# Kernel tuning notes

Measured on AMD Instinct MI355X. Metric: run time of the kernel, lower is better.

The kernel has to match this reference:

```python
import jax, jax.numpy as jnp
import numpy as np

B, N_LAT, N_PAT = 32, 64, 4096
DIM_LAT = DIM_PAT = DIM_ATTN = 192
H = 6
HD = DIM_ATTN // H  # 32
SCALE = HD ** -0.5


def setup_inputs() -> dict:
    key = jax.random.key(0)
    ks = jax.random.split(key, 8)
    s = lambda fan_in: 1.0 / np.sqrt(fan_in)
    return {
        "x_latents": jax.random.normal(ks[0], (B, N_LAT, DIM_LAT), jnp.float32),
        "x_patches": jax.random.normal(ks[1], (B, N_PAT, DIM_PAT), jnp.float32),
        # weights stored [in, out] (torch Linear applies x @ W.T; math identical)
        "W_rv_lat": jax.random.uniform(ks[2], (DIM_LAT, 2 * DIM_ATTN), jnp.float32, -s(DIM_LAT), s(DIM_LAT)),
        "W_rv_pat": jax.random.uniform(ks[3], (DIM_PAT, 2 * DIM_ATTN), jnp.float32, -s(DIM_PAT), s(DIM_PAT)),
        "W_proj_lat": jax.random.uniform(ks[4], (DIM_ATTN, DIM_LAT), jnp.float32, -s(DIM_ATTN), s(DIM_ATTN)),
        "b_proj_lat": jax.random.uniform(ks[5], (DIM_LAT,), jnp.float32, -s(DIM_ATTN), s(DIM_ATTN)),
        "W_proj_pat": jax.random.uniform(ks[6], (DIM_ATTN, DIM_PAT), jnp.float32, -s(DIM_ATTN), s(DIM_ATTN)),
        "b_proj_pat": jax.random.uniform(ks[7], (DIM_PAT,), jnp.float32, -s(DIM_ATTN), s(DIM_ATTN)),
    }


def _split_rv(x, W, n):
    # x: [B, n, d_in] -> r, v each [B, H, n, HD]
    rv = (x @ W).reshape(x.shape[0], n, 2, H, HD)
    rv = jnp.transpose(rv, (2, 0, 3, 1, 4))  # [2, B, H, n, HD]
    return rv[0], rv[1]


def reference(x_latents, x_patches, W_rv_lat, W_rv_pat,
              W_proj_lat, b_proj_lat, W_proj_pat, b_proj_pat):
    r_lat, v_lat = _split_rv(x_latents, W_rv_lat, N_LAT)   # [B,H,N_lat,HD]
    r_pat, v_pat = _split_rv(x_patches, W_rv_pat, N_PAT)   # [B,H,N_pat,HD]

    # single score matrix, softmaxed along both axes (dropout = 0, eval mode)
    scores = jnp.einsum('bhld,bhpd->bhlp', r_lat, r_pat) * SCALE  # [B,H,N_lat,N_pat]
    attn = jax.nn.softmax(scores, axis=-1)    # row-wise (over patches)
    attn_T = jax.nn.softmax(scores, axis=-2)  # col-wise (over latents)

    out_lat = jnp.einsum('bhlp,bhpd->blhd', attn, v_pat).reshape(B, N_LAT, DIM_ATTN)
    out_pat = jnp.einsum('bhlp,bhld->bphd', attn_T, v_lat).reshape(B, N_PAT, DIM_ATTN)

    out_lat = out_lat @ W_proj_lat + b_proj_lat
    out_pat = out_pat @ W_proj_pat + b_proj_pat
    return out_lat, out_pat
```

## Files before the change

kernel.cpp:

```cpp
#include <hip/hip_runtime.h>

#define B_   32
#define NL_  64
#define NP_  4096
#define DIM_ 192
#define H_   6
#define HD_  32
#define PC_  128
#define NCH_ (NP_/PC_)
#define CPB_ 4
#define NSC_ (NCH_/CPB_)

typedef unsigned short u16;
typedef __attribute__((ext_vector_type(8))) short bf16x8;
typedef __attribute__((ext_vector_type(4))) short bf16x4;
typedef __attribute__((ext_vector_type(4))) float f32x4;

#define MFMA16(a,b,c) __builtin_amdgcn_mfma_f32_16x16x32_bf16(a,b,c,0,0,0)

__device__ __forceinline__ float bf2f(u16 s){ return __builtin_bit_cast(float,(unsigned)s<<16); }
__device__ __forceinline__ u16 f2bf(float f){
  unsigned u = __builtin_bit_cast(unsigned,f);
  return (u16)((u + 0x7FFFu + ((u>>16)&1u))>>16);
}

__global__ void k0_transpose(const float* __restrict__ W0, const float* __restrict__ W1,
                             const float* __restrict__ W2, const float* __restrict__ W3,
                             u16* __restrict__ T0, u16* __restrict__ T1,
                             u16* __restrict__ T2, u16* __restrict__ T3){
  int m = blockIdx.x >> 4, sub = blockIdx.x & 15;
  const float* src; u16* dst; int R, C;
  if      (m==0){src=W0;dst=T0;R=192;C=384;}
  else if (m==1){src=W1;dst=T1;R=192;C=384;}
  else if (m==2){src=W2;dst=T2;R=192;C=192;}
  else          {src=W3;dst=T3;R=192;C=192;}
  int total = R*C;
  for (int o = sub*256 + threadIdx.x; o < total; o += 16*256){
    int c = o / R, r = o - c*R;
    dst[o] = f2bf(src[r*C + c]);
  }
}

__global__ __launch_bounds__(512,2) void k_rv(const float* __restrict__ X,
    const u16* __restrict__ Wt, u16* __restrict__ R, u16* __restrict__ V,
    int Nseq, int nshift){
  __shared__ u16 Bs[2][64*200];
  const int t = threadIdx.x;
  const int m0 = blockIdx.x*256;
  const int lane = t & 63, w = t >> 6, g = lane >> 4, ln = lane & 15;
  const int srB = t >> 3, bq = t & 7;
  const f32x4 ZF = {0.f,0.f,0.f,0.f};

  bf16x8 af[2][6];
  #pragma unroll
  for (int i=0;i<2;i++)
    #pragma unroll
    for (int kk=0;kk<6;kk++){
      const float* s = &X[(size_t)(m0 + w*32 + i*16 + ln)*192 + kk*32 + g*8];
      float4 x0 = *(const float4*)s;
      float4 x1 = *(const float4*)(s+4);
      bf16x8 v;
      v[0]=(short)f2bf(x0.x); v[1]=(short)f2bf(x0.y); v[2]=(short)f2bf(x0.z); v[3]=(short)f2bf(x0.w);
      v[4]=(short)f2bf(x1.x); v[5]=(short)f2bf(x1.y); v[6]=(short)f2bf(x1.z); v[7]=(short)f2bf(x1.w);
      af[i][kk] = v;
    }

  bf16x8 breg[3];
  #pragma unroll
  for (int it=0; it<3; it++)
    breg[it] = *(const bf16x8*)&Wt[(size_t)srB*192 + bq*24 + it*8];
  #pragma unroll
  for (int it=0; it<3; it++)
    *(bf16x8*)&Bs[0][srB*200 + bq*24 + it*8] = breg[it];
  #pragma unroll
  for (int it=0; it<3; it++)
    breg[it] = *(const bf16x8*)&Wt[(size_t)(64 + srB)*192 + bq*24 + it*8];
  __syncthreads();

  for (int c = 0; c < 6; ++c){
    if (c < 5){
      u16* bn = &Bs[(c+1)&1][0];
      #pragma unroll
      for (int it=0; it<3; it++)
        *(bf16x8*)&bn[srB*200 + bq*24 + it*8] = breg[it];
      if (c < 4){
        #pragma unroll
        for (int it=0; it<3; it++)
          breg[it] = *(const bf16x8*)&Wt[(size_t)((c+2)*64 + srB)*192 + bq*24 + it*8];
      }
    }
    const u16* bc = &Bs[c&1][0];
    f32x4 accT[4][2];
    #pragma unroll
    for(int j=0;j<4;j++){ accT[j][0]=ZF; accT[j][1]=ZF; }
    #pragma unroll
    for (int kk=0; kk<6; kk++)
      #pragma unroll
      for (int j=0; j<4; j++){
        bf16x8 bv = *(const bf16x8*)&bc[(j*16 + ln)*200 + kk*32 + g*8];
        accT[j][0] = MFMA16(bv, af[0][kk], accT[j][0]);
        accT[j][1] = MFMA16(bv, af[1][kk], accT[j][1]);
      }
    #pragma unroll
    for(int j=0;j<4;j++){
      int nb = c*64 + j*16 + g*4;
      u16* dst; int cc;
      if (nb < 192){ dst = R; cc = nb; } else { dst = V; cc = nb - 192; }
      int h = cc >> 5, d0 = cc & 31;
      #pragma unroll
      for(int i=0;i<2;i++){
        int m = m0 + w*32 + i*16 + ln;
        int b = m >> nshift, sidx = m & (Nseq-1);
        bf16x4 pk;
        #pragma unroll
        for(int r=0;r<4;r++) pk[r] = (short)f2bf(accT[j][i][r]);
        *(bf16x4*)&dst[((((size_t)b*H_ + h)*(size_t)Nseq + sidx) << 5) + d0] = pk;
      }
    }
    __syncthreads();
  }
}

__global__ __launch_bounds__(256) void k_attn(
    const u16* __restrict__ r_lat_g, const u16* __restrict__ v_lat_g,
    const u16* __restrict__ r_pat_g, const u16* __restrict__ v_pat_g,
    u16* __restrict__ Opat,
    float* __restrict__ numT_ws,
    float* __restrict__ rowsum_ws){
  const float SCALE = 0.17677669529663687f;
  const int sc = blockIdx.x, h = blockIdx.y, b = blockIdx.z;
  const int bh = b*H_ + h;
  const int t = threadIdx.x, lane = t&63, w = t>>6, g = lane>>4, ln = lane&15;
  __shared__ u16 RL [64*40];
  __shared__ u16 VLT[32*72];
  __shared__ u16 EN [128*72];
  __shared__ u16 ET [64*136];
  __shared__ float RS[4*64];
  __shared__ u16 POOL[128*40];
  u16* RP  = POOL;
  u16* VPT = POOL;
  const f32x4 ZF = {0.f,0.f,0.f,0.f};

  const size_t latbase = (size_t)bh * (NL_*HD_);
  { int row = t>>2, col = (t&3)*8;
    *(bf16x8*)&RL[row*40+col] = *(const bf16x8*)&r_lat_g[latbase + row*32 + col]; }
  { int l = t>>2, dd = (t&3)*8;
    bf16x8 v = *(const bf16x8*)&v_lat_g[latbase + l*32 + dd];
    #pragma unroll
    for(int jj=0;jj<8;jj++) VLT[(dd+jj)*72 + l] = (u16)v[jj]; }

  const int p0 = t>>2, dd0 = (t&3)*8;
  const size_t pb0 = ((size_t)bh*NP_ + (size_t)sc*(CPB_*PC_))*HD_;
  bf16x8 rcur0 = *(const bf16x8*)&r_pat_g[pb0 + (size_t)p0*32 + dd0];
  bf16x8 rcur1 = *(const bf16x8*)&r_pat_g[pb0 + (size_t)(64+p0)*32 + dd0];
  bf16x8 vcur0 = *(const bf16x8*)&v_pat_g[pb0 + (size_t)p0*32 + dd0];
  bf16x8 vcur1 = *(const bf16x8*)&v_pat_g[pb0 + (size_t)(64+p0)*32 + dd0];

  f32x4 nmT[2]; nmT[0]=ZF; nmT[1]=ZF;
  float rs[4] = {0.f,0.f,0.f,0.f};

  for (int c = 0; c < CPB_; ++c){
    *(bf16x8*)&RP[p0*40 + dd0]      = rcur0;
    *(bf16x8*)&RP[(64+p0)*40 + dd0] = rcur1;
    __syncthreads();

    f32x4 sf[2][4];
    { bf16x8 a0 = *(const bf16x8*)&RP[(w*32      + ln)*40 + g*8];
      bf16x8 a1 = *(const bf16x8*)&RP[(w*32 + 16 + ln)*40 + g*8];
      #pragma unroll
      for(int j=0;j<4;j++){
        bf16x8 bl = *(const bf16x8*)&RL[(j*16 + ln)*40 + g*8];
        sf[0][j] = MFMA16(a0, bl, ZF);
        sf[1][j] = MFMA16(a1, bl, ZF);
      } }

    bf16x8 rnxt0, rnxt1, vnxt0, vnxt1;
    const bool more = (c+1 < CPB_);
    if (more){
      const size_t pbn = pb0 + (size_t)(c+1)*(PC_*HD_);
      rnxt0 = *(const bf16x8*)&r_pat_g[pbn + (size_t)p0*32 + dd0];
      rnxt1 = *(const bf16x8*)&r_pat_g[pbn + (size_t)(64+p0)*32 + dd0];
      vnxt0 = *(const bf16x8*)&v_pat_g[pbn + (size_t)p0*32 + dd0];
      vnxt1 = *(const bf16x8*)&v_pat_g[pbn + (size_t)(64+p0)*32 + dd0];
    }

    float e[2][4][4], rcs[2][4];
    #pragma unroll
    for(int i=0;i<2;i++)
      #pragma unroll
      for(int r=0;r<4;r++){
        float cs = 0.f;
        #pragma unroll
        for(int j=0;j<4;j++){
          float ev = __expf(sf[i][j][r] * SCALE);
          e[i][j][r] = ev; cs += ev; rs[j] += ev;
        }
        cs += __shfl_xor(cs,1); cs += __shfl_xor(cs,2);
        cs += __shfl_xor(cs,4); cs += __shfl_xor(cs,8);
        rcs[i][r] = 1.0f / cs;
      }
    #pragma unroll
    for(int i=0;i<2;i++)
      #pragma unroll
      for(int j=0;j<4;j++){
        #pragma unroll
        for(int r=0;r<4;r++)
          EN[(w*32 + i*16 + g*4 + r)*72 + j*16 + ln] = f2bf(e[i][j][r]*rcs[i][r]);
        bf16x4 pk;
        #pragma unroll
        for(int r=0;r<4;r++) pk[r] = (short)f2bf(e[i][j][r]);
        *(bf16x4*)&ET[(j*16+ln)*136 + w*32 + i*16 + g*4] = pk;
      }

    f32x4 opT[2][2];
    #pragma unroll
    for(int jd=0;jd<2;jd++){ opT[jd][0]=ZF; opT[jd][1]=ZF; }
    #pragma unroll
    for(int ks=0; ks<2; ks++){
      bf16x8 bv[2];
      #pragma unroll
      for(int jd=0;jd<2;jd++) bv[jd] = *(const bf16x8*)&VLT[(jd*16+ln)*72 + ks*32 + g*8];
      #pragma unroll
      for(int i=0;i<2;i++){
        bf16x8 afen = *(const bf16x8*)&EN[(w*32 + i*16 + ln)*72 + ks*32 + g*8];
        #pragma unroll
        for(int jd=0;jd<2;jd++) opT[jd][i] = MFMA16(bv[jd], afen, opT[jd][i]);
      }
    }
    const size_t obase = ((size_t)b*NP_ + (size_t)(sc*CPB_ + c)*PC_)*DIM_ + h*32;
    #pragma unroll
    for(int jd=0;jd<2;jd++)
      #pragma unroll
      for(int i=0;i<2;i++){
        int p = w*32 + i*16 + ln, d0 = jd*16 + g*4;
        bf16x4 pk;
        #pragma unroll
        for(int r=0;r<4;r++) pk[r] = (short)f2bf(opT[jd][i][r]);
        *(bf16x4*)&Opat[obase + (size_t)p*DIM_ + d0] = pk;
      }
    __syncthreads();

    #pragma unroll
    for(int jj=0;jj<8;jj++){
      VPT[(dd0+jj)*136 + p0]      = (u16)vcur0[jj];
      VPT[(dd0+jj)*136 + 64 + p0] = (u16)vcur1[jj];
    }
    __syncthreads();

    #pragma unroll
    for(int ks=0; ks<4; ks++){
      bf16x8 afet = *(const bf16x8*)&ET[(w*16+ln)*136 + ks*32 + g*8];
      #pragma unroll
      for(int dj=0;dj<2;dj++){
        bf16x8 bv = *(const bf16x8*)&VPT[(dj*16+ln)*136 + ks*32 + g*8];
        nmT[dj] = MFMA16(bv, afet, nmT[dj]);
      }
    }
    __syncthreads();

    if (more){ rcur0=rnxt0; rcur1=rnxt1; vcur0=vnxt0; vcur1=vnxt1; }
  }

  #pragma unroll
  for(int j=0;j<4;j++){
    float vs = rs[j];
    vs += __shfl_xor(vs,16); vs += __shfl_xor(vs,32);
    if (g == 0) RS[w*64 + j*16 + ln] = vs;
  }
  __syncthreads();
  if (t < 64)
    rowsum_ws[((size_t)bh*NSC_ + sc)*64 + t] = RS[t] + RS[64+t] + RS[128+t] + RS[192+t];
  float* dstN = numT_ws + ((size_t)bh*NSC_ + sc)*2048;
  #pragma unroll
  for(int dj=0;dj<2;dj++){
    int l = w*16 + ln, d0 = dj*16 + g*4;
    *(f32x4*)&dstN[l*32 + d0] = nmT[dj];
  }
}

__global__ __launch_bounds__(256) void k_lat_reduce(const float* __restrict__ numT_ws,
    const float* __restrict__ rowsum_ws, u16* __restrict__ attn_lat){
  int bh = blockIdx.x, b = bh / H_, h = bh - b*H_;
  __shared__ float RSs[64];
  int t = threadIdx.x;
  if (t < 64){
    float s = 0.f;
    for(int c=0;c<NSC_;c++) s += rowsum_ws[((size_t)bh*NSC_ + c)*64 + t];
    RSs[t] = 1.0f / s;
  }
  __syncthreads();
  for(int idx = t; idx < 2048; idx += 256){
    int l = idx >> 5, dd = idx & 31;
    float s = 0.f;
    for(int c=0;c<NSC_;c++) s += numT_ws[((size_t)bh*NSC_ + c)*2048 + idx];
    attn_lat[((size_t)b*NL_ + l)*DIM_ + h*32 + dd] = f2bf(s * RSs[l]);
  }
}

__global__ __launch_bounds__(256) void k_proj_lat(const u16* __restrict__ A,
    const u16* __restrict__ Wt, const float* __restrict__ bias, float* __restrict__ out){
  int b = blockIdx.x;
  __shared__ u16 As[64*40];
  __shared__ u16 Bs[192*40];
  int t = threadIdx.x, lane = t&63, w = t>>6, g = lane>>4, ln = lane&15;
  const f32x4 ZF = {0.f,0.f,0.f,0.f};
  f32x4 acc[4][3];
  #pragma unroll
  for(int i=0;i<4;i++)
    #pragma unroll
    for(int j=0;j<3;j++) acc[i][j]=ZF;
  for(int k0=0;k0<192;k0+=32){
    bf16x8 av; bf16x8 bv[3];
    { int row = t>>2, col=(t&3)*8;
      av = *(const bf16x8*)&A[((size_t)b*NL_ + row)*DIM_ + k0 + col]; }
    #pragma unroll
    for(int it=0;it<3;it++){
      int e = it*2048 + t*8, row = e>>5, col = (t&3)*8;
      bv[it] = *(const bf16x8*)&Wt[(size_t)row*192 + k0 + col];
    }
    if (k0) __syncthreads();
    { int row = t>>2, col=(t&3)*8; *(bf16x8*)&As[row*40+col] = av; }
    #pragma unroll
    for(int it=0;it<3;it++){
      int e = it*2048 + t*8, row = e>>5, col = (t&3)*8;
      *(bf16x8*)&Bs[row*40+col] = bv[it];
    }
    __syncthreads();
    bf16x8 bw[3];
    #pragma unroll
    for(int jf=0;jf<3;jf++) bw[jf] = *(const bf16x8*)&Bs[(w*48 + jf*16 + ln)*40 + g*8];
    #pragma unroll
    for(int lf=0;lf<4;lf++){
      bf16x8 af = *(const bf16x8*)&As[(lf*16 + ln)*40 + g*8];
      #pragma unroll
      for(int jf=0;jf<3;jf++) acc[lf][jf] = MFMA16(af, bw[jf], acc[lf][jf]);
    }
  }
  #pragma unroll
  for(int lf=0;lf<4;lf++)
    #pragma unroll
    for(int jf=0;jf<3;jf++){
      int j = w*48 + jf*16 + ln;
      float bs = bias[j];
      #pragma unroll
      for(int r=0;r<4;r++){
        int l = lf*16 + g*4 + r;
        out[((size_t)b*NL_ + l)*DIM_ + j] = acc[lf][jf][r] + bs;
      }
    }
}

__global__ __launch_bounds__(512,2) void k_proj_pat(const u16* __restrict__ X,
    const u16* __restrict__ Wt, const float* __restrict__ bias, float* __restrict__ out){
  __shared__ u16 Bs[2][64*200];
  const int t = threadIdx.x;
  const int m0 = blockIdx.x*256;
  const int lane = t & 63, w = t >> 6, g = lane >> 4, ln = lane & 15;
  const int srB = t >> 3, bq = t & 7;
  const f32x4 ZF = {0.f,0.f,0.f,0.f};

  bf16x8 af[2][6];
  #pragma unroll
  for (int i=0;i<2;i++)
    #pragma unroll
    for (int kk=0;kk<6;kk++)
      af[i][kk] = *(const bf16x8*)&X[(size_t)(m0 + w*32 + i*16 + ln)*192 + kk*32 + g*8];

  bf16x8 breg[3];
  #pragma unroll
  for (int it=0; it<3; it++)
    breg[it] = *(const bf16x8*)&Wt[(size_t)srB*192 + bq*24 + it*8];
  #pragma unroll
  for (int it=0; it<3; it++)
    *(bf16x8*)&Bs[0][srB*200 + bq*24 + it*8] = breg[it];
  #pragma unroll
  for (int it=0; it<3; it++)
    breg[it] = *(const bf16x8*)&Wt[(size_t)(64 + srB)*192 + bq*24 + it*8];
  __syncthreads();

  for (int c = 0; c < 3; ++c){
    if (c < 2){
      u16* bn = &Bs[(c+1)&1][0];
      #pragma unroll
      for (int it=0; it<3; it++)
        *(bf16x8*)&bn[srB*200 + bq*24 + it*8] = breg[it];
      if (c < 1){
        #pragma unroll
        for (int it=0; it<3; it++)
          breg[it] = *(const bf16x8*)&Wt[(size_t)((c+2)*64 + srB)*192 + bq*24 + it*8];
      }
    }
    const u16* bc = &Bs[c&1][0];
    f32x4 accT[4][2];
    #pragma unroll
    for(int j=0;j<4;j++){ accT[j][0]=ZF; accT[j][1]=ZF; }
    #pragma unroll
    for (int kk=0; kk<6; kk++)
      #pragma unroll
      for (int j=0; j<4; j++){
        bf16x8 bv = *(const bf16x8*)&bc[(j*16 + ln)*200 + kk*32 + g*8];
        accT[j][0] = MFMA16(bv, af[0][kk], accT[j][0]);
        accT[j][1] = MFMA16(bv, af[1][kk], accT[j][1]);
      }
    #pragma unroll
    for(int j=0;j<4;j++){
      int nb = c*64 + j*16 + g*4;
      float4 bs4 = *(const float4*)&bias[nb];
      #pragma unroll
      for(int i=0;i<2;i++){
        int m = m0 + w*32 + i*16 + ln;
        float4 o;
        o.x = accT[j][i][0] + bs4.x;
        o.y = accT[j][i][1] + bs4.y;
        o.z = accT[j][i][2] + bs4.z;
        o.w = accT[j][i][3] + bs4.w;
        *(float4*)&out[(size_t)m*192 + nb] = o;
      }
    }
    __syncthreads();
  }
}

extern "C" void kernel_launch(void* const* d_in, const int* in_sizes, int n_in,
                              void* d_out, int out_size, void* d_ws, size_t ws_size,
                              hipStream_t stream){
  const float* x_lat  = (const float*)d_in[0];
  const float* x_pat  = (const float*)d_in[1];
  const float* W_rv_l = (const float*)d_in[2];
  const float* W_rv_p = (const float*)d_in[3];
  const float* W_pj_l = (const float*)d_in[4];
  const float* b_pj_l = (const float*)d_in[5];
  const float* W_pj_p = (const float*)d_in[6];
  const float* b_pj_p = (const float*)d_in[7];
  float* out = (float*)d_out;

  char* ws = (char*)d_ws;
  size_t off = 0;
  auto alloc = [&](size_t bytes)->void*{ void* p = ws + off; off += (bytes + 255) & ~(size_t)255; return p; };
  u16* WtRL   = (u16*)alloc((size_t)384*192*2);
  u16* WtRP   = (u16*)alloc((size_t)384*192*2);
  u16* WtPL   = (u16*)alloc((size_t)192*192*2);
  u16* WtPP   = (u16*)alloc((size_t)192*192*2);
  u16* r_lat  = (u16*)alloc((size_t)B_*H_*NL_*HD_*2);
  u16* v_lat  = (u16*)alloc((size_t)B_*H_*NL_*HD_*2);
  u16* r_pat  = (u16*)alloc((size_t)B_*H_*NP_*HD_*2);
  u16* v_pat  = (u16*)alloc((size_t)B_*H_*NP_*HD_*2);
  u16* Opat   = (u16*)alloc((size_t)B_*NP_*DIM_*2);
  float* numT = (float*)alloc((size_t)B_*H_*NSC_*64*32*4);
  float* rsum = (float*)alloc((size_t)B_*H_*NSC_*64*4);
  u16* attn_l = (u16*)alloc((size_t)B_*NL_*DIM_*2);

  k0_transpose<<<64,256,0,stream>>>(W_rv_l, W_rv_p, W_pj_l, W_pj_p, WtRL, WtRP, WtPL, WtPP);
  k_rv<<<dim3((B_*NP_)/256),512,0,stream>>>(x_pat, WtRP, r_pat, v_pat, NP_, 12);
  k_rv<<<dim3((B_*NL_)/256),512,0,stream>>>(x_lat, WtRL, r_lat, v_lat, NL_, 6);
  k_attn<<<dim3(NSC_, H_, B_),256,0,stream>>>(r_lat, v_lat, r_pat, v_pat, Opat, numT, rsum);
  k_lat_reduce<<<B_*H_,256,0,stream>>>(numT, rsum, attn_l);
  k_proj_lat<<<B_,256,0,stream>>>(attn_l, WtPL, b_pj_l, out);
  k_proj_pat<<<dim3((B_*NP_)/256),512,0,stream>>>(Opat, WtPP, b_pj_p, out + (size_t)B_*NL_*DIM_);
}
```

Before: 177.4 us.

## Pre-swizzle weights into MFMA fragment order and read them directly from global

The weight transpose kernel now writes the rv and patch-projection weights in the exact per-lane MFMA fragment order, so each lane loads its B-operand with one contiguous 16-byte global read. The LDS double-buffering, staging loads and per-chunk barriers in k_rv and k_proj_pat are removed. Blocks shrink to 256 threads covering 128 rows, with 4 blocks per CU. This removes shared-memory traffic and synchronisation, but every wave now re-reads the small weight matrix from L1/L2 instead of sharing one LDS copy.

```diff
diff --git a/kernel.cpp b/kernel.cpp
--- a/kernel.cpp
+++ b/kernel.cpp
@@ -29,26 +29,34 @@
                              u16* __restrict__ T0, u16* __restrict__ T1,
                              u16* __restrict__ T2, u16* __restrict__ T3){
   int m = blockIdx.x >> 4, sub = blockIdx.x & 15;
-  const float* src; u16* dst; int R, C;
-  if      (m==0){src=W0;dst=T0;R=192;C=384;}
-  else if (m==1){src=W1;dst=T1;R=192;C=384;}
-  else if (m==2){src=W2;dst=T2;R=192;C=192;}
-  else          {src=W3;dst=T3;R=192;C=192;}
-  int total = R*C;
+  if (m == 2){
+    for (int o = sub*256 + threadIdx.x; o < 192*192; o += 16*256){
+      int n = o / 192, k = o - n*192;
+      T2[o] = f2bf(W2[k*192 + n]);
+    }
+    return;
+  }
+  const float* src; u16* dst; int NF, C;
+  if      (m==0){src=W0;dst=T0;NF=144;C=384;}
+  else if (m==1){src=W1;dst=T1;NF=144;C=384;}
+  else          {src=W3;dst=T3;NF=72; C=192;}
+  int total = NF*512;
   for (int o = sub*256 + threadIdx.x; o < total; o += 16*256){
-    int c = o / R, r = o - c*R;
-    dst[o] = f2bf(src[r*C + c]);
-  }
-}
-
-__global__ __launch_bounds__(512,2) void k_rv(const float* __restrict__ X,
-    const u16* __restrict__ Wt, u16* __restrict__ R, u16* __restrict__ V,
+    int e = o & 7, l = (o >> 3) & 63, f = o >> 9;
+    int kk = f % 6, jc = f / 6;
+    int j = jc & 3, c = jc >> 2;
+    int n = c*64 + j*16 + (l & 15);
+    int k = kk*32 + (l >> 4)*8 + e;
+    dst[o] = f2bf(src[k*C + n]);
+  }
+}
+
+__global__ __launch_bounds__(256,4) void k_rv(const float* __restrict__ X,
+    const u16* __restrict__ Wf, u16* __restrict__ R, u16* __restrict__ V,
     int Nseq, int nshift){
-  __shared__ u16 Bs[2][64*200];
   const int t = threadIdx.x;
-  const int m0 = blockIdx.x*256;
+  const int m0 = blockIdx.x*128;
   const int lane = t & 63, w = t >> 6, g = lane >> 4, ln = lane & 15;
-  const int srB = t >> 3, bq = t & 7;
   const f32x4 ZF = {0.f,0.f,0.f,0.f};
 
   bf16x8 af[2][6];
@@ -65,31 +73,7 @@
       af[i][kk] = v;
     }
 
-  bf16x8 breg[3];
-  #pragma unroll
-  for (int it=0; it<3; it++)
-    breg[it] = *(const bf16x8*)&Wt[(size_t)srB*192 + bq*24 + it*8];
-  #pragma unroll
-  for (int it=0; it<3; it++)
-    *(bf16x8*)&Bs[0][srB*200 + bq*24 + it*8] = breg[it];
-  #pragma unroll
-  for (int it=0; it<3; it++)
-    breg[it] = *(const bf16x8*)&Wt[(size_t)(64 + srB)*192 + bq*24 + it*8];
-  __syncthreads();
-
   for (int c = 0; c < 6; ++c){
-    if (c < 5){
-      u16* bn = &Bs[(c+1)&1][0];
-      #pragma unroll
-      for (int it=0; it<3; it++)
-        *(bf16x8*)&bn[srB*200 + bq*24 + it*8] = breg[it];
-      if (c < 4){
-        #pragma unroll
-        for (int it=0; it<3; it++)
-          breg[it] = *(const bf16x8*)&Wt[(size_t)((c+2)*64 + srB)*192 + bq*24 + it*8];
-      }
-    }
-    const u16* bc = &Bs[c&1][0];
     f32x4 accT[4][2];
     #pragma unroll
     for(int j=0;j<4;j++){ accT[j][0]=ZF; accT[j][1]=ZF; }
@@ -97,7 +81,7 @@
     for (int kk=0; kk<6; kk++)
       #pragma unroll
       for (int j=0; j<4; j++){
-        bf16x8 bv = *(const bf16x8*)&bc[(j*16 + ln)*200 + kk*32 + g*8];
+        bf16x8 bv = *(const bf16x8*)&Wf[(size_t)(((c*4 + j)*6 + kk) << 9) + lane*8];
         accT[j][0] = MFMA16(bv, af[0][kk], accT[j][0]);
         accT[j][1] = MFMA16(bv, af[1][kk], accT[j][1]);
       }
@@ -117,7 +101,6 @@
         *(bf16x4*)&dst[((((size_t)b*H_ + h)*(size_t)Nseq + sidx) << 5) + d0] = pk;
       }
     }
-    __syncthreads();
   }
 }
 
@@ -350,13 +333,11 @@
     }
 }
 
-__global__ __launch_bounds__(512,2) void k_proj_pat(const u16* __restrict__ X,
-    const u16* __restrict__ Wt, const float* __restrict__ bias, float* __restrict__ out){
-  __shared__ u16 Bs[2][64*200];
+__global__ __launch_bounds__(256,4) void k_proj_pat(const u16* __restrict__ X,
+    const u16* __restrict__ Wf, const float* __restrict__ bias, float* __restrict__ out){
   const int t = threadIdx.x;
-  const int m0 = blockIdx.x*256;
+  const int m0 = blockIdx.x*128;
   const int lane = t & 63, w = t >> 6, g = lane >> 4, ln = lane & 15;
-  const int srB = t >> 3, bq = t & 7;
   const f32x4 ZF = {0.f,0.f,0.f,0.f};
 
   bf16x8 af[2][6];
@@ -366,31 +347,7 @@
     for (int kk=0;kk<6;kk++)
       af[i][kk] = *(const bf16x8*)&X[(size_t)(m0 + w*32 + i*16 + ln)*192 + kk*32 + g*8];
 
-  bf16x8 breg[3];
-  #pragma unroll
-  for (int it=0; it<3; it++)
-    breg[it] = *(const bf16x8*)&Wt[(size_t)srB*192 + bq*24 + it*8];
-  #pragma unroll
-  for (int it=0; it<3; it++)
-    *(bf16x8*)&Bs[0][srB*200 + bq*24 + it*8] = breg[it];
-  #pragma unroll
-  for (int it=0; it<3; it++)
-    breg[it] = *(const bf16x8*)&Wt[(size_t)(64 + srB)*192 + bq*24 + it*8];
-  __syncthreads();
-
   for (int c = 0; c < 3; ++c){
-    if (c < 2){
-      u16* bn = &Bs[(c+1)&1][0];
-      #pragma unroll
-      for (int it=0; it<3; it++)
-        *(bf16x8*)&bn[srB*200 + bq*24 + it*8] = breg[it];
-      if (c < 1){
-        #pragma unroll
-        for (int it=0; it<3; it++)
-          breg[it] = *(const bf16x8*)&Wt[(size_t)((c+2)*64 + srB)*192 + bq*24 + it*8];
-      }
-    }
-    const u16* bc = &Bs[c&1][0];
     f32x4 accT[4][2];
     #pragma unroll
     for(int j=0;j<4;j++){ accT[j][0]=ZF; accT[j][1]=ZF; }
@@ -398,7 +355,7 @@
     for (int kk=0; kk<6; kk++)
       #pragma unroll
       for (int j=0; j<4; j++){
-        bf16x8 bv = *(const bf16x8*)&bc[(j*16 + ln)*200 + kk*32 + g*8];
+        bf16x8 bv = *(const bf16x8*)&Wf[(size_t)(((c*4 + j)*6 + kk) << 9) + lane*8];
         accT[j][0] = MFMA16(bv, af[0][kk], accT[j][0]);
         accT[j][1] = MFMA16(bv, af[1][kk], accT[j][1]);
       }
@@ -417,7 +374,6 @@
         *(float4*)&out[(size_t)m*192 + nb] = o;
       }
     }
-    __syncthreads();
   }
 }
 
@@ -437,10 +393,10 @@
   char* ws = (char*)d_ws;
   size_t off = 0;
   auto alloc = [&](size_t bytes)->void*{ void* p = ws + off; off += (bytes + 255) & ~(size_t)255; return p; };
-  u16* WtRL   = (u16*)alloc((size_t)384*192*2);
-  u16* WtRP   = (u16*)alloc((size_t)384*192*2);
+  u16* WtRL   = (u16*)alloc((size_t)144*512*2);
+  u16* WtRP   = (u16*)alloc((size_t)144*512*2);
   u16* WtPL   = (u16*)alloc((size_t)192*192*2);
-  u16* WtPP   = (u16*)alloc((size_t)192*192*2);
+  u16* WtPP   = (u16*)alloc((size_t)72*512*2);
   u16* r_lat  = (u16*)alloc((size_t)B_*H_*NL_*HD_*2);
   u16* v_lat  = (u16*)alloc((size_t)B_*H_*NL_*HD_*2);
   u16* r_pat  = (u16*)alloc((size_t)B_*H_*NP_*HD_*2);
@@ -451,10 +407,10 @@
   u16* attn_l = (u16*)alloc((size_t)B_*NL_*DIM_*2);
 
   k0_transpose<<<64,256,0,stream>>>(W_rv_l, W_rv_p, W_pj_l, W_pj_p, WtRL, WtRP, WtPL, WtPP);
-  k_rv<<<dim3((B_*NP_)/256),512,0,stream>>>(x_pat, WtRP, r_pat, v_pat, NP_, 12);
-  k_rv<<<dim3((B_*NL_)/256),512,0,stream>>>(x_lat, WtRL, r_lat, v_lat, NL_, 6);
+  k_rv<<<dim3((B_*NP_)/128),256,0,stream>>>(x_pat, WtRP, r_pat, v_pat, NP_, 12);
+  k_rv<<<dim3((B_*NL_)/128),256,0,stream>>>(x_lat, WtRL, r_lat, v_lat, NL_, 6);
   k_attn<<<dim3(NSC_, H_, B_),256,0,stream>>>(r_lat, v_lat, r_pat, v_pat, Opat, numT, rsum);
   k_lat_reduce<<<B_*H_,256,0,stream>>>(numT, rsum, attn_l);
   k_proj_lat<<<B_,256,0,stream>>>(attn_l, WtPL, b_pj_l, out);
-  k_proj_pat<<<dim3((B_*NP_)/256),512,0,stream>>>(Opat, WtPP, b_pj_p, out + (size_t)B_*NL_*DIM_);
-}
+  k_proj_pat<<<dim3((B_*NP_)/128),256,0,stream>>>(Opat, WtPP, b_pj_p, out + (size_t)B_*NL_*DIM_);
+}
```

New measurement: 198.4 us. +11.8%, slower.
